# Optimization experiments

Hardware: AMD Instinct MI355X
Metric: run time of the kernel (lower is better)

## Reference

```python
import jax, jax.numpy as jnp
import numpy as np

B, T, D, H, QK, V, M = 2, 2048, 1024, 16, 64, 64, 1024
SOFTCAP = 50.0


def apply_rope(x, positions, max_wavelength=10000.0):
    # x: (B, T, H, d), positions: (T,)
    d = x.shape[-1]
    fraction = 2.0 * jnp.arange(d // 2, dtype=jnp.float32) / d
    timescale = max_wavelength ** fraction                      # (d/2,)
    sinusoid = positions.astype(jnp.float32)[:, None] / timescale  # (T, d/2)
    sin = jnp.sin(sinusoid)[:, None, :]  # (T, 1, d/2) broadcasts over heads
    cos = jnp.cos(sinusoid)[:, None, :]
    x1, x2 = jnp.split(x, 2, axis=-1)
    out = jnp.concatenate([x1 * cos - x2 * sin, x2 * cos + x1 * sin], axis=-1)
    return out.astype(x.dtype)


def rms_norm(x, scale, eps=1e-6):
    var = jnp.mean(jnp.square(x.astype(jnp.float32)), axis=-1, keepdims=True)
    normed = x * jax.lax.rsqrt(var + eps).astype(x.dtype)
    return normed * (1.0 + scale).astype(x.dtype)


def setup_inputs() -> dict:
    key = jax.random.key(0)
    ks = jax.random.split(key, 10)
    s = 0.02
    # key-padding mask: per-batch kv valid lengths (all rows have >=1536 valid keys)
    kv_lens = jnp.array([1536, 2048], dtype=jnp.int32)
    mask = (jnp.arange(T)[None, :] < kv_lens[:, None])  # (B, Tk)
    mask = jnp.broadcast_to(mask[:, None, None, :], (B, 1, T, T))
    return {
        "q": jax.random.normal(ks[0], (B, T, D), jnp.float32),
        "kv": jax.random.normal(ks[1], (B, T, D), jnp.float32),
        "mask": mask,
        "q_positions": jnp.arange(T, dtype=jnp.int32),
        "kv_positions": jnp.arange(T, dtype=jnp.int32),
        "wq": jax.random.normal(ks[2], (D, H * QK), jnp.float32) * s,
        "bq": jnp.zeros((H * QK,), jnp.float32),
        "wk": jax.random.normal(ks[3], (D, H * QK), jnp.float32) * s,
        "bk": jnp.zeros((H * QK,), jnp.float32),
        "wv": jax.random.normal(ks[4], (D, H * V), jnp.float32) * s,
        "bv": jnp.zeros((H * V,), jnp.float32),
        "q_scale": jnp.zeros((QK,), jnp.float32),
        "k_scale": jnp.zeros((QK,), jnp.float32),
        "wo": jax.random.normal(ks[5], (H * V, M), jnp.float32) * s,
        "bo": jnp.zeros((M,), jnp.float32),
    }


def reference(q, kv, mask, q_positions, kv_positions,
              wq, bq, wk, bk, wv, bv, q_scale, k_scale, wo, bo):
    qh = (q @ wq + bq).reshape(B, T, H, QK)
    kh = (kv @ wk + bk).reshape(B, T, H, QK)
    vh = (kv @ wv + bv).reshape(B, T, H, V)
    # QK RMSNorm
    qh = rms_norm(qh, q_scale)
    kh = rms_norm(kh, k_scale)
    # RoPE
    qh = apply_rope(qh, q_positions)
    kh = apply_rope(kh, kv_positions)
    # softcapped, masked attention
    logits = jnp.einsum("bthd,bThd->bhtT", qh, kh) / np.sqrt(QK).astype(jnp.float32)
    logits = SOFTCAP * jnp.tanh(logits / SOFTCAP)
    logits = jnp.where(mask, logits, -1e9)
    log_probs = jax.nn.log_softmax(logits, axis=-1)
    probs = jnp.exp(log_probs)
    probs = jnp.where(mask, probs, 0.0)
    # normalized attention entropy (B, H, T)
    entropy = -jnp.sum(probs * log_probs, axis=-1) / jnp.log(mask.sum(axis=-1))
    attn = jnp.einsum("bhtT,bThd->bthd", probs, vh).reshape(B, T, H * V)
    out = attn @ wo + bo
    return out, entropy
```

## Files before the change

### kernel.cpp

```cpp
#include <hip/hip_runtime.h>

#define BB 2
#define TT 2048
#define DD 1024
#define HH 16
#define QKD 64
#define VD 64
#define MD 1024

typedef _Float16 half4 __attribute__((ext_vector_type(4)));
typedef _Float16 half8 __attribute__((ext_vector_type(8)));
typedef __fp16 fp16x2 __attribute__((ext_vector_type(2)));
typedef float f32x4 __attribute__((ext_vector_type(4)));
typedef unsigned short us8 __attribute__((ext_vector_type(8)));
typedef unsigned short us4 __attribute__((ext_vector_type(4)));

__device__ __forceinline__ unsigned short f2h(float x){
    union { _Float16 h; unsigned short u; } c; c.h = (_Float16)x; return c.u;
}

__device__ __forceinline__ void gl16(const void* g, void* l){
    __builtin_amdgcn_global_load_lds(
        (const __attribute__((address_space(1))) void*)g,
        (__attribute__((address_space(3))) void*)l, 16, 0, 0);
}

__global__ __launch_bounds__(256) void k_prep(const float* __restrict__ q,
                                              const float* __restrict__ kv,
                                              unsigned short* __restrict__ q_bf,
                                              unsigned short* __restrict__ kv_bf,
                                              const float* __restrict__ w0,
                                              const float* __restrict__ w1,
                                              const float* __restrict__ w2,
                                              const float* __restrict__ w3,
                                              unsigned short* __restrict__ o0,
                                              unsigned short* __restrict__ o1,
                                              unsigned short* __restrict__ o2,
                                              unsigned short* __restrict__ o3,
                                              const int* __restrict__ qpos,
                                              const int* __restrict__ kpos,
                                              float* __restrict__ tabq,
                                              float* __restrict__ tabk,
                                              const unsigned char* __restrict__ mask,
                                              int* __restrict__ kvlen){
    __shared__ float smem[64*65];
    int bid = blockIdx.x, tid = threadIdx.x;
    if (bid < 8192){
        const int n = BB*TT*DD/4;
        int idx = bid*256 + tid;
        const float* src = (idx < n) ? q : kv;
        unsigned short* dst = (idx < n) ? q_bf : kv_bf;
        int i = ((idx < n) ? idx : idx - n)*4;
        const float4 v = *(const float4*)(src + i);
        us4 o; o.x = f2h(v.x); o.y = f2h(v.y); o.z = f2h(v.z); o.w = f2h(v.w);
        *(us4*)(dst + i) = o;
    } else if (bid < 9216){
        int idx2 = bid - 8192;
        int z = idx2 >> 8;
        int rc2 = idx2 & 255;
        const float* in = (z==0) ? w0 : (z==1) ? w1 : (z==2) ? w2 : w3;
        unsigned short* out = (z==0) ? o0 : (z==1) ? o1 : (z==2) ? o2 : o3;
        float (*ts)[65] = (float(*)[65])smem;
        int r0 = (rc2 & 15)*64, c0 = (rc2 >> 4)*64;
        int lr = tid >> 4, lc = (tid & 15)*4;
#pragma unroll
        for (int i = 0; i < 4; ++i){
            const float4 v = *(const float4*)(in + (long)(r0 + lr + i*16)*1024 + c0 + lc);
            ts[lr+i*16][lc+0] = v.x; ts[lr+i*16][lc+1] = v.y;
            ts[lr+i*16][lc+2] = v.z; ts[lr+i*16][lc+3] = v.w;
        }
        __syncthreads();
        int oc = tid >> 2, rc = (tid & 3)*16;
        int ocp = oc;
        if (z < 2){
            int blk = oc >> 4;
            ocp = (blk == 1) ? oc + 16 : ((blk == 2) ? oc - 16 : oc);
        }
        us8 o0v, o1v;
#pragma unroll
        for (int j = 0; j < 8; ++j){ o0v[j] = f2h(ts[rc+j][ocp]); o1v[j] = f2h(ts[rc+8+j][ocp]); }
        *(us8*)(out + (long)(c0+oc)*1024 + r0 + rc)     = o0v;
        *(us8*)(out + (long)(c0+oc)*1024 + r0 + rc + 8) = o1v;
    } else if (bid < 9728){
        int gi = (bid - 9216)*256 + tid;
        const int* pos = (gi < 65536) ? qpos : kpos;
        float* tab = (gi < 65536) ? tabq : tabk;
        int idx = gi & 65535;
        int t = idx >> 5, f = idx & 31;
        float invts = expf(-((float)f*(1.f/32.f)) * 9.210340371976184f);
        float ph = (float)pos[t]*invts;
        ((float2*)tab)[idx] = make_float2(sinf(ph), cosf(ph));
    } else {
        int* red = (int*)smem;
        int b = bid - 9728;
        bool bytemode = (mask[1] != 0);
        int cnt = 0;
        for (int j = tid; j < TT; j += 256){
            long e = (long)b*TT*TT + j;
            if (bytemode) cnt += (mask[e] != 0);
            else          cnt += (((const unsigned int*)mask)[e] != 0);
        }
        red[tid] = cnt; __syncthreads();
        for (int s = 128; s > 0; s >>= 1){ if (tid < s) red[tid] += red[tid+s]; __syncthreads(); }
        if (tid == 0) kvlen[b] = red[0];
    }
}

#define GEMM_CORE(A_, Bt_, abase, bbase)                                            \
    int srow = l >> 3;                                                              \
    int scol = ((l & 7) ^ srow)*8;                                                  \
    int swb = lg ^ (li & 7);                                                        \
    const unsigned short* ga[4]; const unsigned short* gb[2];                       \
    _Pragma("unroll")                                                               \
    for (int i = 0; i < 4; ++i) ga[i] = A_  + (long)(m0 + w*32 + i*8 + srow)*1024 + scol; \
    _Pragma("unroll")                                                               \
    for (int i = 0; i < 2; ++i) gb[i] = Bt_ + (long)(n0 + w*16 + i*8 + srow)*1024 + scol; \
    _Pragma("unroll")                                                               \
    for (int i = 0; i < 4; ++i) gl16(ga[i], abase + (w*32 + i*8)*128);              \
    _Pragma("unroll")                                                               \
    for (int i = 0; i < 2; ++i) gl16(gb[i], bbase + (w*16 + i*8)*128);              \
    __syncthreads();                                                                \
    for (int ks = 0; ks < 16; ++ks){                                                \
        int cur = ks & 1;                                                           \
        if (ks + 1 < 16){                                                           \
            char* an = abase + (cur^1)*16384;                                       \
            char* bn = bbase + (cur^1)*8192;                                        \
            _Pragma("unroll")                                                       \
            for (int i = 0; i < 4; ++i){ ga[i] += 64; gl16(ga[i], an + (w*32 + i*8)*128); } \
            _Pragma("unroll")                                                       \
            for (int i = 0; i < 2; ++i){ gb[i] += 64; gl16(gb[i], bn + (w*16 + i*8)*128); } \
        }                                                                           \
        const char* ac = abase + cur*16384;                                         \
        const char* bc = bbase + cur*8192;                                          \
        _Pragma("unroll")                                                           \
        for (int kk = 0; kk < 2; ++kk){                                             \
            int co = ((kk*4) ^ swb)*16;                                             \
            half8 af[4], bf[2];                                                     \
            _Pragma("unroll")                                                       \
            for (int mi = 0; mi < 4; ++mi) af[mi] = *(const half8*)(ac + (wm + mi*16 + li)*128 + co); \
            _Pragma("unroll")                                                       \
            for (int ni = 0; ni < 2; ++ni) bf[ni] = *(const half8*)(bc + (wn + ni*16 + li)*128 + co); \
            _Pragma("unroll")                                                       \
            for (int mi = 0; mi < 4; ++mi)                                          \
                _Pragma("unroll")                                                   \
                for (int ni = 0; ni < 2; ++ni)                                      \
                    acc[mi][ni] = __builtin_amdgcn_mfma_f32_16x16x32_f16(af[mi], bf[ni], acc[mi][ni], 0, 0, 0); \
        }                                                                           \
        __syncthreads();                                                            \
    }

__global__ __launch_bounds__(256) void k_gemm3(const unsigned short* __restrict__ q_bf,
                                               const unsigned short* __restrict__ kv_bf,
                                               const unsigned short* __restrict__ wqt,
                                               const unsigned short* __restrict__ wkt,
                                               const unsigned short* __restrict__ wvt,
                                               const float* __restrict__ bq,
                                               const float* __restrict__ bk,
                                               const float* __restrict__ bv,
                                               const float* __restrict__ qscale,
                                               const float* __restrict__ kscale,
                                               const float* __restrict__ tabq,
                                               const float* __restrict__ tabk,
                                               unsigned short* __restrict__ Qr,
                                               unsigned short* __restrict__ Kr,
                                               unsigned short* __restrict__ VTb){
    __shared__ float4 smem_[3072];
    char* abase = (char*)smem_;
    char* bbase = abase + 32768;
    int flat = blockIdx.x;
    int virt = (flat & 7)*192 + (flat >> 3);
    int z = virt >> 9;
    int rem = virt & 511;
    int m0 = (rem >> 4)*128;
    int nx = rem & 15;
    int n0 = nx*64;
    const unsigned short* A  = (z == 0) ? q_bf : kv_bf;
    const unsigned short* Bt = (z == 0) ? wqt : (z == 1) ? wkt : wvt;

    int tid = threadIdx.x, l = tid & 63, w = tid >> 6;
    int lg = l >> 4, li = l & 15;
    int wm = (w >> 1)*64, wn = (w & 1)*32;
    f32x4 zero = {0.f,0.f,0.f,0.f};
    f32x4 acc[4][2];
#pragma unroll
    for (int mi = 0; mi < 4; ++mi){ acc[mi][0] = zero; acc[mi][1] = zero; }
    GEMM_CORE(A, Bt, abase, bbase)

    int hd = nx;
    if (z < 2){
        const float* bias  = (z == 0) ? bq : bk;
        const float* scale = (z == 0) ? qscale : kscale;
        const float* tab   = (z == 0) ? tabq : tabk;
        unsigned short* out = (z == 0) ? Qr : Kr;
        float* hs = (float*)smem_;
        int d0 = (wn >> 1) + li;
        float b0 = bias[hd*64 + d0];
        float b1 = bias[hd*64 + d0 + 32];
        float ssp[4][4];
#pragma unroll
        for (int mi = 0; mi < 4; ++mi)
#pragma unroll
            for (int r = 0; r < 4; ++r){
                float x0 = acc[mi][0][r] + b0;
                float x1 = acc[mi][1][r] + b1;
                ssp[mi][r] = x0*x0 + x1*x1;
            }
#pragma unroll
        for (int m = 1; m < 16; m <<= 1)
#pragma unroll
            for (int mi = 0; mi < 4; ++mi)
#pragma unroll
                for (int r = 0; r < 4; ++r) ssp[mi][r] += __shfl_xor(ssp[mi][r], m);
        if (li == 0){
#pragma unroll
            for (int mi = 0; mi < 4; ++mi)
#pragma unroll
                for (int r = 0; r < 4; ++r)
                    hs[(wm + mi*16 + lg*4 + r)*2 + (w & 1)] = ssp[mi][r];
        }
        __syncthreads();
        float sc0 = 1.f + scale[d0];
        float sc1 = 1.f + scale[d0 + 32];
#pragma unroll
        for (int mi = 0; mi < 4; ++mi)
#pragma unroll
            for (int r = 0; r < 4; ++r){
                int row = wm + mi*16 + lg*4 + r;
                float ss = hs[row*2] + hs[row*2 + 1];
                float rstd = rsqrtf(ss*(1.f/64.f) + 1e-6f);
                float x0 = (acc[mi][0][r] + b0)*rstd*sc0;
                float x1 = (acc[mi][1][r] + b1)*rstd*sc1;
                int gm = m0 + row;
                int bb = gm >> 11, t = gm & 2047;
                float2 scv = ((const float2*)tab)[t*32 + d0];
                float o0 = x0*scv.y - x1*scv.x;
                float o1 = x1*scv.y + x0*scv.x;
                long obase = ((long)(bb*HH + hd)*TT + t)*64;
                out[obase + d0]      = f2h(o0);
                out[obase + d0 + 32] = f2h(o1);
            }
    } else {
        float* Tt = (float*)smem_;
#pragma unroll
        for (int mi = 0; mi < 4; ++mi)
#pragma unroll
            for (int ni = 0; ni < 2; ++ni){
                int col = wn + ni*16 + li;
                float bb = bv[hd*64 + col];
#pragma unroll
                for (int r = 0; r < 4; ++r)
                    Tt[col*133 + wm + mi*16 + lg*4 + r] = acc[mi][ni][r] + bb;
            }
        __syncthreads();
        int bb2 = m0 >> 11, t0 = m0 & 2047;
        int vd = tid >> 2, sg = (tid & 3)*32;
        long ob = ((long)(bb2*HH + hd)*64 + vd)*TT + t0 + sg;
#pragma unroll
        for (int c = 0; c < 4; ++c){
            us8 o;
#pragma unroll
            for (int j = 0; j < 8; ++j) o[j] = f2h(Tt[vd*133 + sg + c*8 + j]);
            *(us8*)(VTb + ob + c*8) = o;
        }
    }
}

__global__ __launch_bounds__(256) void k_gemm(const unsigned short* __restrict__ A,
                                              const unsigned short* __restrict__ Bt,
                                              const float* __restrict__ bias,
                                              float* __restrict__ C, int N){
    __shared__ float4 smem_[3072];
    char* abase = (char*)smem_;
    char* bbase = abase + 32768;
    int flat = blockIdx.x;
    int virt = (flat & 7)*64 + (flat >> 3);
    int m0 = (virt >> 4)*128, n0 = (virt & 15)*64;
    int tid = threadIdx.x, l = tid & 63, w = tid >> 6;
    int lg = l >> 4, li = l & 15;
    int wm = (w >> 1)*64, wn = (w & 1)*32;
    f32x4 zero = {0.f,0.f,0.f,0.f};
    f32x4 acc[4][2];
#pragma unroll
    for (int mi = 0; mi < 4; ++mi){ acc[mi][0] = zero; acc[mi][1] = zero; }
    GEMM_CORE(A, Bt, abase, bbase)
#pragma unroll
    for (int mi = 0; mi < 4; ++mi){
#pragma unroll
        for (int ni = 0; ni < 2; ++ni){
            int row = m0 + wm + mi*16 + lg*4;
            int col = n0 + wn + ni*16 + li;
            float bb = bias[col];
#pragma unroll
            for (int r = 0; r < 4; ++r)
                C[(long)(row + r)*N + col] = acc[mi][ni][r] + bb;
        }
    }
}

#define ATTN_SMPV(I_, SACC_)                                                        \
    {                                                                               \
        float xs2[4][4];                                                            \
        bool tail = ((I_)*64 + 64 > kvl);                                           \
        if (tail){                                                                  \
            _Pragma("unroll")                                                       \
            for (int jt = 0; jt < 4; ++jt){                                         \
                _Pragma("unroll")                                                   \
                for (int r = 0; r < 4; ++r){                                        \
                    float u = SACC_[jt][r];                                         \
                    float z2 = u*u;                                                 \
                    float v = u*(PA + z2*(PB + z2*PC));                             \
                    xs2[jt][r] = ((I_)*64 + jt*16 + lg*4 + r < kvl) ? v : -1e30f;   \
                }                                                                   \
            }                                                                       \
        } else {                                                                    \
            _Pragma("unroll")                                                       \
            for (int jt = 0; jt < 4; ++jt){                                         \
                _Pragma("unroll")                                                   \
                for (int r = 0; r < 4; ++r){                                        \
                    float u = SACC_[jt][r];                                         \
                    float z2 = u*u;                                                 \
                    xs2[jt][r] = u*(PA + z2*(PB + z2*PC));                          \
                }                                                                   \
            }                                                                       \
        }                                                                           \
        float p[4][4];                                                              \
        _Pragma("unroll")                                                           \
        for (int jt = 0; jt < 4; ++jt){                                             \
            _Pragma("unroll")                                                       \
            for (int r = 0; r < 4; ++r){                                            \
                float pp = exp2f(xs2[jt][r]);                                       \
                p[jt][r] = pp;                                                      \
                l4[r]  += pp;                                                       \
                s14[r] += pp * xs2[jt][r];                                          \
            }                                                                       \
        }                                                                           \
        half4 pa[4];                                                                \
        _Pragma("unroll")                                                           \
        for (int kk = 0; kk < 4; ++kk){                                             \
            union { half4 v; fp16x2 h2[2]; } up;                                    \
            up.h2[0] = __builtin_amdgcn_cvt_pkrtz(p[kk][0], p[kk][1]);              \
            up.h2[1] = __builtin_amdgcn_cvt_pkrtz(p[kk][2], p[kk][3]);              \
            pa[kk] = up.v;                                                          \
        }                                                                           \
        const char* vc = vsb + ((I_) & 1)*8192;                                     \
        _Pragma("unroll")                                                           \
        for (int kk = 0; kk < 4; ++kk){                                             \
            int co = (((kk*2) ^ swb))*16 + off8;                                    \
            _Pragma("unroll")                                                       \
            for (int jv = 0; jv < 4; ++jv){                                         \
                half4 vf = *(const half4*)(vc + (jv*16 + li)*128 + co);             \
                oacc[jv] = __builtin_amdgcn_mfma_f32_16x16x16f16(pa[kk], vf, oacc[jv], 0, 0, 0); \
            }                                                                       \
        }                                                                           \
    }

__global__ __launch_bounds__(512) void k_attn(const unsigned short* __restrict__ Qr,
                                              const unsigned short* __restrict__ Kr,
                                              const unsigned short* __restrict__ VT,
                                              const int* __restrict__ kvlen,
                                              unsigned short* __restrict__ attnb,
                                              float* __restrict__ ent){
    __shared__ unsigned short Ks[2][64][64];
    __shared__ unsigned short Vs[2][64][64];
    int tid = threadIdx.x;
    int l = tid & 63, w = tid >> 6;
    int lg = l >> 4, li = l & 15;
    int flat = blockIdx.x;
    int xcd = flat & 7;
    int idx = flat >> 3;
    int qt = idx & 15;
    int g = idx >> 4;
    int bh = xcd*2 + (g & 1) + (g >> 1)*16;
    int b = bh >> 4, h = bh & 15;
    long qk0 = (long)bh * TT * 64;
    long vt0 = (long)bh * 64 * TT;
    int kvl = kvlen[b];
    int q0 = qt*128 + w*16;

    half8 qf[2];
#pragma unroll
    for (int kk = 0; kk < 2; ++kk)
        qf[kk] = *(const half8*)(Qr + qk0 + (long)(q0 + li)*64 + kk*32 + lg*8);

    int r0s = tid >> 3;
    int kcs = (tid & 7)*8;
    int sws = (((tid & 7) ^ (r0s & 7)))*16;
    char* ksb = (char*)Ks;
    char* vsb = (char*)Vs;
    int swb = (lg >> 1) ^ (li & 7);
    int off8 = (lg & 1)*8;

    f32x4 zero = {0.f,0.f,0.f,0.f};
    f32x4 oacc[4];
#pragma unroll
    for (int jv = 0; jv < 4; ++jv) oacc[jv] = zero;
    float l4[4]  = {0.f,0.f,0.f,0.f};
    float s14[4] = {0.f,0.f,0.f,0.f};

    const float PA = 0.18033688f;
    const float PB = -3.7570183e-7f;
    const float PC = 9.3925458e-13f;

    int nkv = (kvl + 63) >> 6;

    {
        us8 ka = *(const us8*)(Kr + qk0 + (long)r0s*64 + kcs);
        us8 va = *(const us8*)(VT + vt0 + (long)r0s*TT + kcs);
        *(us8*)(ksb + r0s*128 + sws) = ka;
        *(us8*)(vsb + r0s*128 + sws) = va;
    }
    __syncthreads();
    f32x4 scur[4];
#pragma unroll
    for (int jt = 0; jt < 4; ++jt) scur[jt] = zero;
#pragma unroll
    for (int kk = 0; kk < 2; ++kk){
        int co = ((kk*4 + lg) ^ (li & 7))*16;
#pragma unroll
        for (int jt = 0; jt < 4; ++jt){
            half8 kf = *(const half8*)(ksb + (jt*16 + li)*128 + co);
            scur[jt] = __builtin_amdgcn_mfma_f32_16x16x32_f16(kf, qf[kk], scur[jt], 0, 0, 0);
        }
    }
    {
        us8 ka = *(const us8*)(Kr + qk0 + (long)(64 + r0s)*64 + kcs);
        *(us8*)(ksb + 8192 + r0s*128 + sws) = ka;
    }
    __syncthreads();

    for (int i = 0; i < nkv - 1; ++i){
        int cur = i & 1;
        us8 ka, va;
        bool pk = (i + 2 < nkv);
        if (pk) ka = *(const us8*)(Kr + qk0 + (long)((i+2)*64 + r0s)*64 + kcs);
        va = *(const us8*)(VT + vt0 + (long)r0s*TT + (i+1)*64 + kcs);
        const char* kc = ksb + ((i+1) & 1)*8192;
        f32x4 snext[4];
#pragma unroll
        for (int jt = 0; jt < 4; ++jt) snext[jt] = zero;
#pragma unroll
        for (int kk = 0; kk < 2; ++kk){
            int co = ((kk*4 + lg) ^ (li & 7))*16;
#pragma unroll
            for (int jt = 0; jt < 4; ++jt){
                half8 kf = *(const half8*)(kc + (jt*16 + li)*128 + co);
                snext[jt] = __builtin_amdgcn_mfma_f32_16x16x32_f16(kf, qf[kk], snext[jt], 0, 0, 0);
            }
        }
        ATTN_SMPV(i, scur)
        if (pk) *(us8*)(ksb + cur*8192 + r0s*128 + sws) = ka;
        *(us8*)(vsb + ((i+1) & 1)*8192 + r0s*128 + sws) = va;
        __syncthreads();
#pragma unroll
        for (int jt = 0; jt < 4; ++jt) scur[jt] = snext[jt];
    }
    {
        int i = nkv - 1;
        ATTN_SMPV(i, scur)
    }

    float l_r  = (l4[0] + l4[1]) + (l4[2] + l4[3]);
    float s1_r = (s14[0] + s14[1]) + (s14[2] + s14[3]);
    l_r  += __shfl_xor(l_r, 16);  l_r  += __shfl_xor(l_r, 32);
    s1_r += __shfl_xor(s1_r, 16); s1_r += __shfl_xor(s1_r, 32);

    float invl = 1.f / l_r;
    float invr[4];
#pragma unroll
    for (int r = 0; r < 4; ++r) invr[r] = __shfl(invl, lg*4 + r);
#pragma unroll
    for (int jv = 0; jv < 4; ++jv){
#pragma unroll
        for (int r = 0; r < 4; ++r){
            int qrow = q0 + lg*4 + r;
            attnb[((long)b*TT + qrow)*1024 + h*64 + jv*16 + li] = f2h(oacc[jv][r]*invr[r]);
        }
    }
    if (l < 16){
        const float LN2 = 0.6931471805599453f;
        float lse = logf(l_r);
        float s1n = s1_r*LN2;
        ent[(long)bh*TT + q0 + li] = (lse - s1n*invl) / logf((float)kvl);
    }
}

extern "C" void kernel_launch(void* const* d_in, const int* in_sizes, int n_in,
                              void* d_out, int out_size, void* d_ws, size_t ws_size,
                              hipStream_t stream){
    (void)in_sizes; (void)n_in; (void)out_size; (void)ws_size;
    const float* q      = (const float*)d_in[0];
    const float* kv     = (const float*)d_in[1];
    const unsigned char* mask = (const unsigned char*)d_in[2];
    const int*   qpos   = (const int*)d_in[3];
    const int*   kpos   = (const int*)d_in[4];
    const float* wq     = (const float*)d_in[5];
    const float* bq     = (const float*)d_in[6];
    const float* wk     = (const float*)d_in[7];
    const float* bk     = (const float*)d_in[8];
    const float* wv     = (const float*)d_in[9];
    const float* bv     = (const float*)d_in[10];
    const float* qscale = (const float*)d_in[11];
    const float* kscale = (const float*)d_in[12];
    const float* wo     = (const float*)d_in[13];
    const float* bo     = (const float*)d_in[14];
    float* out = (float*)d_out;
    float* ent = out + (long)BB*TT*MD;

    char* ws = (char*)d_ws;
    unsigned short* wqt   = (unsigned short*)(ws);
    unsigned short* wkt   = (unsigned short*)(ws + 2097152L);
    unsigned short* wvt   = (unsigned short*)(ws + 4194304L);
    unsigned short* wot   = (unsigned short*)(ws + 6291456L);
    unsigned short* q_bf  = (unsigned short*)(ws + 8388608L);
    unsigned short* kv_bf = (unsigned short*)(ws + 16777216L);
    unsigned short* Qr    = (unsigned short*)(ws + 25165824L);
    unsigned short* Kr    = (unsigned short*)(ws + 33554432L);
    unsigned short* VTb   = (unsigned short*)(ws + 41943040L);
    unsigned short* attnb = (unsigned short*)(ws + 50331648L);
    float*          tabq  = (float*)(ws + 58720256L);
    float*          tabk  = (float*)(ws + 59244544L);
    int*            kvln  = (int*)(ws + 59768832L);

    k_prep<<<9730, 256, 0, stream>>>(q, kv, q_bf, kv_bf,
                                     wq, wk, wv, wo, wqt, wkt, wvt, wot,
                                     qpos, kpos, tabq, tabk, mask, kvln);

    k_gemm3<<<1536, 256, 0, stream>>>(q_bf, kv_bf, wqt, wkt, wvt,
                                      bq, bk, bv, qscale, kscale,
                                      tabq, tabk, Qr, Kr, VTb);

    k_attn<<<512, 512, 0, stream>>>(Qr, Kr, VTb, kvln, attnb, ent);

    k_gemm<<<512, 256, 0, stream>>>(attnb, wot, bo, out, 1024);
}
```

Measured before the change: 135.9 us.

## Split attention KV range across two blocks and combine partials in new kernel

```diff
diff --git a/kernel.cpp b/kernel.cpp
--- a/kernel.cpp
+++ b/kernel.cpp
@@ -17,6 +17,9 @@
 
 __device__ __forceinline__ unsigned short f2h(float x){
     union { _Float16 h; unsigned short u; } c; c.h = (_Float16)x; return c.u;
+}
+__device__ __forceinline__ float h2f(unsigned short x){
+    union { unsigned short u; _Float16 h; } c; c.u = x; return (float)c.h;
 }
 
 __device__ __forceinline__ void gl16(const void* g, void* l){
@@ -297,7 +300,7 @@
     }
 }
 
-#define ATTN_SMPV(I_, SACC_)                                                        \
+#define ATTN_SMPV(I_, J_, SACC_)                                                    \
     {                                                                               \
         float xs2[4][4];                                                            \
         bool tail = ((I_)*64 + 64 > kvl);                                           \
@@ -342,7 +345,7 @@
             up.h2[1] = __builtin_amdgcn_cvt_pkrtz(p[kk][2], p[kk][3]);              \
             pa[kk] = up.v;                                                          \
         }                                                                           \
-        const char* vc = vsb + ((I_) & 1)*8192;                                     \
+        const char* vc = vsb + ((J_) & 1)*8192;                                     \
         _Pragma("unroll")                                                           \
         for (int kk = 0; kk < 4; ++kk){                                             \
             int co = (((kk*2) ^ swb))*16 + off8;                                    \
@@ -358,8 +361,10 @@
                                               const unsigned short* __restrict__ Kr,
                                               const unsigned short* __restrict__ VT,
                                               const int* __restrict__ kvlen,
-                                              unsigned short* __restrict__ attnb,
-                                              float* __restrict__ ent){
+                                              unsigned short* __restrict__ O0,
+                                              unsigned short* __restrict__ O1,
+                                              float* __restrict__ lp,
+                                              float* __restrict__ s1p){
     __shared__ unsigned short Ks[2][64][64];
     __shared__ unsigned short Vs[2][64][64];
     int tid = threadIdx.x;
@@ -369,7 +374,8 @@
     int xcd = flat & 7;
     int idx = flat >> 3;
     int qt = idx & 15;
-    int g = idx >> 4;
+    int g = (idx >> 4) & 3;
+    int half = idx >> 6;
     int bh = xcd*2 + (g & 1) + (g >> 1)*16;
     int b = bh >> 4, h = bh & 15;
     long qk0 = (long)bh * TT * 64;
@@ -402,10 +408,12 @@
     const float PC = 9.3925458e-13f;
 
     int nkv = (kvl + 63) >> 6;
+    int t0 = half ? (nkv >> 1) : 0;
+    int t1 = half ? nkv : (nkv >> 1);
 
     {
-        us8 ka = *(const us8*)(Kr + qk0 + (long)r0s*64 + kcs);
-        us8 va = *(const us8*)(VT + vt0 + (long)r0s*TT + kcs);
+        us8 ka = *(const us8*)(Kr + qk0 + (long)(t0*64 + r0s)*64 + kcs);
+        us8 va = *(const us8*)(VT + vt0 + (long)r0s*TT + t0*64 + kcs);
         *(us8*)(ksb + r0s*128 + sws) = ka;
         *(us8*)(vsb + r0s*128 + sws) = va;
     }
@@ -423,18 +431,19 @@
         }
     }
     {
-        us8 ka = *(const us8*)(Kr + qk0 + (long)(64 + r0s)*64 + kcs);
+        us8 ka = *(const us8*)(Kr + qk0 + (long)((t0+1)*64 + r0s)*64 + kcs);
         *(us8*)(ksb + 8192 + r0s*128 + sws) = ka;
     }
     __syncthreads();
 
-    for (int i = 0; i < nkv - 1; ++i){
-        int cur = i & 1;
+    int nloc = t1 - t0;
+    for (int j = 0; j < nloc - 1; ++j){
+        int i = t0 + j;
         us8 ka, va;
-        bool pk = (i + 2 < nkv);
+        bool pk = (i + 2 < t1);
         if (pk) ka = *(const us8*)(Kr + qk0 + (long)((i+2)*64 + r0s)*64 + kcs);
         va = *(const us8*)(VT + vt0 + (long)r0s*TT + (i+1)*64 + kcs);
-        const char* kc = ksb + ((i+1) & 1)*8192;
+        const char* kc = ksb + ((j+1) & 1)*8192;
         f32x4 snext[4];
 #pragma unroll
         for (int jt = 0; jt < 4; ++jt) snext[jt] = zero;
@@ -447,16 +456,16 @@
                 snext[jt] = __builtin_amdgcn_mfma_f32_16x16x32_f16(kf, qf[kk], snext[jt], 0, 0, 0);
             }
         }
-        ATTN_SMPV(i, scur)
-        if (pk) *(us8*)(ksb + cur*8192 + r0s*128 + sws) = ka;
-        *(us8*)(vsb + ((i+1) & 1)*8192 + r0s*128 + sws) = va;
+        ATTN_SMPV(i, j, scur)
+        if (pk) *(us8*)(ksb + (j & 1)*8192 + r0s*128 + sws) = ka;
+        *(us8*)(vsb + ((j+1) & 1)*8192 + r0s*128 + sws) = va;
         __syncthreads();
 #pragma unroll
         for (int jt = 0; jt < 4; ++jt) scur[jt] = snext[jt];
     }
     {
-        int i = nkv - 1;
-        ATTN_SMPV(i, scur)
+        int i = t1 - 1, j = nloc - 1;
+        ATTN_SMPV(i, j, scur)
     }
 
     float l_r  = (l4[0] + l4[1]) + (l4[2] + l4[3]);
@@ -464,23 +473,54 @@
     l_r  += __shfl_xor(l_r, 16);  l_r  += __shfl_xor(l_r, 32);
     s1_r += __shfl_xor(s1_r, 16); s1_r += __shfl_xor(s1_r, 32);
 
-    float invl = 1.f / l_r;
-    float invr[4];
-#pragma unroll
-    for (int r = 0; r < 4; ++r) invr[r] = __shfl(invl, lg*4 + r);
+    unsigned short* Op = half ? O1 : O0;
 #pragma unroll
     for (int jv = 0; jv < 4; ++jv){
 #pragma unroll
         for (int r = 0; r < 4; ++r){
             int qrow = q0 + lg*4 + r;
-            attnb[((long)b*TT + qrow)*1024 + h*64 + jv*16 + li] = f2h(oacc[jv][r]*invr[r]);
+            Op[((long)b*TT + qrow)*1024 + h*64 + jv*16 + li] = f2h(oacc[jv][r]);
         }
     }
     if (l < 16){
-        const float LN2 = 0.6931471805599453f;
-        float lse = logf(l_r);
-        float s1n = s1_r*LN2;
-        ent[(long)bh*TT + q0 + li] = (lse - s1n*invl) / logf((float)kvl);
+        int o = half*65536 + bh*2048 + q0 + li;
+        lp[o]  = l_r;
+        s1p[o] = s1_r;
+    }
+}
+
+__global__ __launch_bounds__(256) void k_comb(const unsigned short* __restrict__ O0,
+                                              const unsigned short* __restrict__ O1,
+                                              const float* __restrict__ lp,
+                                              const float* __restrict__ s1p,
+                                              const int* __restrict__ kvlen,
+                                              unsigned short* __restrict__ attnb,
+                                              float* __restrict__ ent){
+    int bid = blockIdx.x, tid = threadIdx.x;
+    if (bid < 4096){
+        long base = ((long)bid*256 + tid)*4;
+        long row = base >> 10;
+        int hd = (int)(base & 1023);
+        int h = hd >> 6;
+        int b = (int)(row >> 11);
+        int t = (int)(row & 2047);
+        int o = (b*16 + h)*2048 + t;
+        float linv = 1.f / (lp[o] + lp[65536 + o]);
+        us4 a = *(const us4*)(O0 + base);
+        us4 c = *(const us4*)(O1 + base);
+        us4 ov;
+#pragma unroll
+        for (int j = 0; j < 4; ++j)
+            ov[j] = f2h((h2f(a[j]) + h2f(c[j]))*linv);
+        *(us4*)(attnb + base) = ov;
+    } else {
+        int idx = (bid - 4096)*256 + tid;
+        int bh = idx >> 11;
+        int b = bh >> 4;
+        float lsum = lp[idx] + lp[65536 + idx];
+        float ssum = s1p[idx] + s1p[65536 + idx];
+        float invl = 1.f / lsum;
+        ent[idx] = (logf(lsum) - ssum*0.6931471805599453f*invl) / logf((float)kvlen[b]);
     }
 }
 
@@ -520,6 +560,8 @@
     float*          tabq  = (float*)(ws + 58720256L);
     float*          tabk  = (float*)(ws + 59244544L);
     int*            kvln  = (int*)(ws + 59768832L);
+    float*          lp    = (float*)(ws + 59772928L);
+    float*          s1p   = (float*)(ws + 60297216L);
 
     k_prep<<<9730, 256, 0, stream>>>(q, kv, q_bf, kv_bf,
                                      wq, wk, wv, wo, wqt, wkt, wvt, wot,
@@ -529,7 +571,9 @@
                                       bq, bk, bv, qscale, kscale,
                                       tabq, tabk, Qr, Kr, VTb);
 
-    k_attn<<<512, 512, 0, stream>>>(Qr, Kr, VTb, kvln, attnb, ent);
+    k_attn<<<1024, 512, 0, stream>>>(Qr, Kr, VTb, kvln, q_bf, kv_bf, lp, s1p);
+
+    k_comb<<<4352, 256, 0, stream>>>(q_bf, kv_bf, lp, s1p, kvln, attnb, ent);
 
     k_gemm<<<512, 256, 0, stream>>>(attnb, wot, bo, out, 1024);
 }
```

Result: slower. 141.8 us (+4.3%).
